# Kernel tuning notes

Hardware: AMD Instinct MI355X
Metric: run time of the kernel (lower is better)

Reference implementation:

```python
import jax, jax.numpy as jnp
import numpy as np

N, E = 20000, 320000
SQRT3 = float(np.sqrt(3.0))


def setup_inputs() -> dict:
    key = jax.random.key(0)
    ks = jax.random.split(key, 15)
    inp = {
        'node_features': jax.random.normal(ks[0], (N, 128), jnp.float32),
        'node_attrs': jax.random.uniform(ks[1], (N, 4), jnp.float32),
        'edge_attrs': jax.random.normal(ks[2], (E, 4), jnp.float32),
        'edge_embeddings': jax.random.uniform(ks[3], (E, 8), jnp.float32),
        'lin1_w0': jax.random.normal(ks[4], (32, 32), jnp.float32),
        'lin1_w1': jax.random.normal(ks[5], (32, 32), jnp.float32),
        'fc_w1': jax.random.normal(ks[6], (8, 64), jnp.float32),
        'fc_w2': jax.random.normal(ks[7], (64, 64), jnp.float32),
        'fc_w3': jax.random.normal(ks[8], (64, 128), jnp.float32),
        'lin2_w0': jax.random.normal(ks[9], (64, 64), jnp.float32),
        'lin2_w1': jax.random.normal(ks[10], (64, 32), jnp.float32),
        'sc_w0': jax.random.normal(ks[11], (32, 4, 64), jnp.float32),
        'sc_w1': jax.random.normal(ks[12], (32, 4, 32), jnp.float32),
        'edge_index': jax.random.randint(ks[13], (2, E), 0, N),
        'avg_num_neighbors': 16,
    }
    return inp


def reference(node_features, node_attrs, edge_attrs, edge_embeddings,
              lin1_w0, lin1_w1, fc_w1, fc_w2, fc_w3, lin2_w0, lin2_w1,
              sc_w0, sc_w1, edge_index, avg_num_neighbors):
    n = node_features.shape[0]
    src, dst = edge_index[0], edge_index[1]
    # split node features: 32x0e scalars + 32x1o vectors
    x0 = node_features[:, :32]                      # [N,32]
    x1 = node_features[:, 32:].reshape(n, 32, 3)    # [N,32,3]

    # self-connection: FullyConnectedTensorProduct with 4x0e node attrs ('uvw')
    sc_norm = 1.0 / np.sqrt(32 * 4)
    sc0 = jnp.einsum('nu,nv,uvw->nw', x0, node_attrs, sc_w0) * sc_norm   # [N,64]
    sc1 = jnp.einsum('nui,nv,uvw->nwi', x1, node_attrs, sc_w1) * sc_norm  # [N,32,3]

    # linear_1 (per-l equivariant linear, fan-in normalized)
    y0 = (x0 @ lin1_w0) / np.sqrt(32)
    y1 = jnp.einsum('nui,uw->nwi', x1, lin1_w1) / np.sqrt(32)

    # radial MLP -> per-edge TP weights (e3nn FullyConnectedNet: no bias, 1/sqrt(fan_in))
    h = jax.nn.silu((edge_embeddings @ fc_w1) / np.sqrt(8))
    h = jax.nn.silu((h @ fc_w2) / np.sqrt(64))
    w = (h @ fc_w3) / np.sqrt(64)                   # [E,128]
    # weights ordered by instruction: (0ex0e->0e),(0ex1o->1o),(1ox0e->1o),(1ox1o->0e)
    w00, w01, w10, w11 = w[:, :32], w[:, 32:64], w[:, 64:96], w[:, 96:128]

    # gather source node features per edge
    g0 = y0[src]                                    # [E,32]
    g1 = y1[src]                                    # [E,32,3]
    e0 = edge_attrs[:, :1]                          # [E,1]  (0e)
    e1 = edge_attrs[:, 1:4]                         # [E,3]  (1o)

    # sparse CG tensor product, 'uvu' with mul_v=1; output slots sorted as
    # [32x0e (0ex0e), 32x0e (1ox1o), 32x1o (0ex1o), 32x1o (1ox0e)]
    o_s0 = w00 * g0 * e0                                            # [E,32]
    o_s1 = w11 * jnp.einsum('eui,ei->eu', g1, e1) / SQRT3           # [E,32]
    o_v0 = (w01 * g0)[:, :, None] * e1[:, None, :]                  # [E,32,3]
    o_v1 = w10[:, :, None] * g1 * e0[:, :, None]                    # [E,32,3]
    edge_feat = jnp.concatenate(
        [o_s0, o_s1, o_v0.reshape(-1, 96), o_v1.reshape(-1, 96)], axis=1)  # [E,256]

    # scatter-sum into destination nodes
    m = jax.ops.segment_sum(edge_feat, dst, num_segments=n)
    m = m / np.sqrt(float(avg_num_neighbors))

    # linear_2: 64x0e+64x1o -> 64x0e+32x1o
    s0 = m[:, :64]
    s1 = m[:, 64:].reshape(n, 64, 3)
    out0 = (s0 @ lin2_w0) / np.sqrt(64) + sc0       # [N,64]
    out1 = jnp.einsum('nui,uw->nwi', s1, lin2_w1) / np.sqrt(64) + sc1  # [N,32,3]

    # Gate: 32x0e scalars (silu) + 32x0e gates (silu) acting on 32x1o
    scal = jax.nn.silu(out0[:, :32])
    gates = jax.nn.silu(out0[:, 32:])
    vec = gates[:, :, None] * out1                  # [N,32,3]
    new_x = jnp.concatenate([scal, vec.reshape(n, 96)], axis=1)  # [N,128]

    # resnet (irreps_layer_out == irreps_in)
    return node_features + new_x
```

## Files before the change

kernel.cpp:

```cpp
#include <hip/hip_runtime.h>
#include <math.h>

__device__ __forceinline__ float silu(float x) { return x / (1.0f + __expf(-x)); }

typedef __attribute__((ext_vector_type(8))) short short8v;
typedef __attribute__((ext_vector_type(4))) float f32x4;

__device__ __forceinline__ unsigned short f2bf(float x) {
  unsigned int u = __float_as_uint(x);
  return (unsigned short)((u + 0x8000u) >> 16);
}

__global__ __launch_bounds__(256) void node_pre_kernel(
    const float* __restrict__ nf, const float* __restrict__ na,
    const float* __restrict__ w0, const float* __restrict__ w1,
    const float* __restrict__ scw0, const float* __restrict__ scw1,
    float* __restrict__ y, float* __restrict__ sc, int N)
{
  __shared__ float nfL[32][132];
  __shared__ __align__(16) char aB[4096];
  __shared__ __align__(16) char wB[32768];
  const int t = threadIdx.x;
  const int n0 = blockIdx.x * 32;
  const int wv = t >> 6, l = t & 63;
  const int lrow = l & 15, lkg = l >> 4;
  const int ann = t >> 3, ac = t & 7;
  const float inv_sqrt32 = 0.17677669529663687f;
  const float sc_norm    = 0.08838834764831843f;

  for (int x4 = t; x4 < 1024; x4 += 256) {
    const int nn = x4 >> 5, c4 = x4 & 31;
    const int n = n0 + nn;
    float4 v = make_float4(0.f, 0.f, 0.f, 0.f);
    if (n < N) v = *(const float4*)(nf + (size_t)n * 128 + c4 * 4);
    *(float4*)&nfL[nn][c4 * 4] = v;
  }
  if (t < 128) {
    const int nn = t >> 2, c = t & 3;
    const int n = n0 + nn;
    nfL[nn][128 + c] = (n < N) ? na[(size_t)n * 4 + c] : 0.f;
  }
  for (int x = t; x < 1024; x += 256) {
    const int u = x >> 5, w = x & 31;
    *(unsigned short*)(wB + 0 + w * 128 + (((u >> 3) ^ (w & 7)) * 16) + (u & 7) * 2) = f2bf(w0[x]);
  }
  for (int x = t; x < 1024; x += 256) {
    const int u = x >> 5, w = x & 31;
    *(unsigned short*)(wB + 4096 + w * 128 + (((u >> 3) ^ (w & 7)) * 16) + (u & 7) * 2) = f2bf(w1[x]);
  }
  for (int x = t; x < 8192; x += 256) {
    const int k = x >> 6, c = x & 63;
    const int half = k >> 6, kk = k & 63;
    *(unsigned short*)(wB + 8192 + half * 8192 + c * 128 + (((kk >> 3) ^ (c & 7)) * 16) + (kk & 7) * 2) = f2bf(scw0[x]);
  }
  for (int x = t; x < 4096; x += 256) {
    const int k = x >> 5, c = x & 31;
    const int half = k >> 6, kk = k & 63;
    *(unsigned short*)(wB + 24576 + half * 4096 + c * 128 + (((kk >> 3) ^ (c & 7)) * 16) + (kk & 7) * 2) = f2bf(scw1[x]);
  }
  __syncthreads();

  if (ac < 4) {
    short8v hv;
#pragma unroll
    for (int j = 0; j < 8; ++j) hv[j] = (short)f2bf(nfL[ann][ac * 8 + j]);
    *(short8v*)(aB + ann * 128 + ((ac ^ (ann & 7)) * 16));
    *(short8v*)(aB + ann * 128 + ((ac ^ (ann & 7)) * 16)) = hv;
  }
  __syncthreads();
  {
    const int mt = wv >> 1, nt = wv & 1;
    const int ar = mt * 16 + lrow, br = nt * 16 + lrow;
    const short8v A = *(const short8v*)(aB + ar * 128 + ((lkg ^ (ar & 7)) * 16));
    const short8v B = *(const short8v*)(wB + 0 + br * 128 + ((lkg ^ (br & 7)) * 16));
    f32x4 acc = (f32x4){0.f, 0.f, 0.f, 0.f};
    acc = __builtin_amdgcn_mfma_f32_16x16x32_bf16(A, B, acc, 0, 0, 0);
#pragma unroll
    for (int r = 0; r < 4; ++r) {
      const int nn = mt * 16 + lkg * 4 + r;
      const int n = n0 + nn;
      if (n < N) y[(size_t)n * 128 + nt * 16 + lrow] = acc[r] * inv_sqrt32;
    }
  }
  __syncthreads();

  for (int i = 0; i < 3; ++i) {
    if (ac < 4) {
      short8v hv;
#pragma unroll
      for (int j = 0; j < 8; ++j)
        hv[j] = (short)f2bf(nfL[ann][32 + (ac * 8 + j) * 3 + i]);
      *(short8v*)(aB + ann * 128 + ((ac ^ (ann & 7)) * 16)) = hv;
    }
    __syncthreads();
    {
      const int mt = wv >> 1, nt = wv & 1;
      const int ar = mt * 16 + lrow, br = nt * 16 + lrow;
      const short8v A = *(const short8v*)(aB + ar * 128 + ((lkg ^ (ar & 7)) * 16));
      const short8v B = *(const short8v*)(wB + 4096 + br * 128 + ((lkg ^ (br & 7)) * 16));
      f32x4 acc = (f32x4){0.f, 0.f, 0.f, 0.f};
      acc = __builtin_amdgcn_mfma_f32_16x16x32_bf16(A, B, acc, 0, 0, 0);
#pragma unroll
      for (int r = 0; r < 4; ++r) {
        const int nn = mt * 16 + lkg * 4 + r;
        const int n = n0 + nn;
        if (n < N) y[(size_t)n * 128 + 32 + (nt * 16 + lrow) * 3 + i] = acc[r] * inv_sqrt32;
      }
    }
    __syncthreads();
  }

  {
    f32x4 accS[2] = {(f32x4){0.f,0.f,0.f,0.f}, (f32x4){0.f,0.f,0.f,0.f}};
    const int mt = wv & 1, ntb = (wv >> 1) * 2;
#pragma unroll
    for (int half = 0; half < 2; ++half) {
      {
        short8v hv;
#pragma unroll
        for (int j = 0; j < 8; ++j) {
          const int k = half * 64 + ac * 8 + j;
          hv[j] = (short)f2bf(nfL[ann][k >> 2] * nfL[ann][128 + (k & 3)]);
        }
        *(short8v*)(aB + ann * 128 + ((ac ^ (ann & 7)) * 16)) = hv;
      }
      __syncthreads();
#pragma unroll
      for (int step = 0; step < 2; ++step) {
        const int ar = mt * 16 + lrow;
        const short8v A = *(const short8v*)(aB + ar * 128 + (((step * 4 + lkg) ^ (ar & 7)) * 16));
#pragma unroll
        for (int q = 0; q < 2; ++q) {
          const int br = (ntb + q) * 16 + lrow;
          const short8v B = *(const short8v*)(wB + 8192 + half * 8192 + br * 128 + (((step * 4 + lkg) ^ (br & 7)) * 16));
          accS[q] = __builtin_amdgcn_mfma_f32_16x16x32_bf16(A, B, accS[q], 0, 0, 0);
        }
      }
      __syncthreads();
    }
#pragma unroll
    for (int q = 0; q < 2; ++q) {
#pragma unroll
      for (int r = 0; r < 4; ++r) {
        const int nn = mt * 16 + lkg * 4 + r;
        const int n = n0 + nn;
        if (n < N) sc[(size_t)n * 160 + (ntb + q) * 16 + lrow] = accS[q][r] * sc_norm;
      }
    }
  }

  for (int i = 0; i < 3; ++i) {
    f32x4 acc = (f32x4){0.f, 0.f, 0.f, 0.f};
    const int mt = wv >> 1, nt = wv & 1;
#pragma unroll
    for (int half = 0; half < 2; ++half) {
      {
        short8v hv;
#pragma unroll
        for (int j = 0; j < 8; ++j) {
          const int k = half * 64 + ac * 8 + j;
          hv[j] = (short)f2bf(nfL[ann][32 + (k >> 2) * 3 + i] * nfL[ann][128 + (k & 3)]);
        }
        *(short8v*)(aB + ann * 128 + ((ac ^ (ann & 7)) * 16)) = hv;
      }
      __syncthreads();
#pragma unroll
      for (int step = 0; step < 2; ++step) {
        const int ar = mt * 16 + lrow;
        const short8v A = *(const short8v*)(aB + ar * 128 + (((step * 4 + lkg) ^ (ar & 7)) * 16));
        const int br = nt * 16 + lrow;
        const short8v B = *(const short8v*)(wB + 24576 + half * 4096 + br * 128 + (((step * 4 + lkg) ^ (br & 7)) * 16));
        acc = __builtin_amdgcn_mfma_f32_16x16x32_bf16(A, B, acc, 0, 0, 0);
      }
      __syncthreads();
    }
#pragma unroll
    for (int r = 0; r < 4; ++r) {
      const int nn = mt * 16 + lkg * 4 + r;
      const int n = n0 + nn;
      if (n < N) sc[(size_t)n * 160 + 64 + (nt * 16 + lrow) * 3 + i] = acc[r] * sc_norm;
    }
  }
}

__global__ __launch_bounds__(256) void hist_kernel(const int* __restrict__ eidx,
                                                   int* __restrict__ counts, int E)
{
  const int e = blockIdx.x * 256 + threadIdx.x;
  if (e < E) atomicAdd(&counts[eidx[E + e]], 1);
}

__global__ __launch_bounds__(1024) void scan_kernel(const int* __restrict__ counts,
                                                    int* __restrict__ offsets,
                                                    int* __restrict__ cursor, int N)
{
  __shared__ int part[1024];
  const int t = threadIdx.x;
  const int per = (N + 1023) / 1024;
  const int base = t * per;
  int s = 0;
  for (int k = 0; k < per; ++k) { int idx = base + k; if (idx < N) s += counts[idx]; }
  part[t] = s;
  __syncthreads();
  for (int off = 1; off < 1024; off <<= 1) {
    int v = part[t];
    if (t >= off) v += part[t - off];
    __syncthreads();
    part[t] = v;
    __syncthreads();
  }
  int run = (t == 0) ? 0 : part[t - 1];
  for (int k = 0; k < per; ++k) {
    int idx = base + k;
    if (idx < N) { offsets[idx] = run; cursor[idx] = run; run += counts[idx]; }
  }
  if (t == 1023) offsets[N] = run;
}

__global__ __launch_bounds__(256) void scatter_kernel(const int* __restrict__ eidx,
                                                      int* __restrict__ cursor,
                                                      int* __restrict__ elist, int E)
{
  const int e = blockIdx.x * 256 + threadIdx.x;
  if (e >= E) return;
  const int dst = eidx[E + e];
  const int slot = atomicAdd(&cursor[dst], 1);
  elist[slot] = e;
}

__global__ __launch_bounds__(256) void edge_mlp_kernel(
    const float* __restrict__ eemb, const float* __restrict__ fw1,
    const float* __restrict__ fw2, const float* __restrict__ fw3,
    const int* __restrict__ elist, float* __restrict__ wbuf, int E)
{
  __shared__ __align__(16) float w1L[512];
  __shared__ __align__(16) char reg1[16384];
  __shared__ __align__(16) char reg2[32768];
  const int t = threadIdx.x;
  const int base = blockIdx.x * 128;

  for (int x = t; x < 512; x += 256)  w1L[x] = fw1[(x & 7) * 64 + (x >> 3)];
  for (int x = t; x < 4096; x += 256) {
    const int k = x >> 6, o = x & 63;
    *(unsigned short*)(reg2 + o * 128 + (((k >> 3) ^ (o & 7)) * 16) + (k & 7) * 2) = f2bf(fw2[x]);
  }

  const int e = t & 127, kg = t >> 7;
  {
    const int slot0 = base + e;
    const int eid = (slot0 < E) ? elist[slot0] : 0;
    const float4 em0 = *(const float4*)(eemb + (size_t)eid * 8);
    const float4 em1 = *(const float4*)(eemb + (size_t)eid * 8 + 4);
    __syncthreads();

    const float inv_sqrt8 = 0.35355339059327373f;
#pragma unroll
    for (int c = 0; c < 4; ++c) {
      short8v hv;
#pragma unroll
      for (int j = 0; j < 8; ++j) {
        const int k = kg * 32 + c * 8 + j;
        const float4 wa = *(const float4*)(w1L + k * 8);
        const float4 wb = *(const float4*)(w1L + k * 8 + 4);
        const float a = em0.x * wa.x + em0.y * wa.y + em0.z * wa.z + em0.w * wa.w
                      + em1.x * wb.x + em1.y * wb.y + em1.z * wb.z + em1.w * wb.w;
        hv[j] = (short)f2bf(silu(a * inv_sqrt8));
      }
      const int cc = kg * 4 + c;
      *(short8v*)(reg1 + e * 128 + ((cc ^ (e & 7)) * 16)) = hv;
    }
  }
  __syncthreads();

  const int wv = t >> 6, l = t & 63;
  const int lrow = l & 15, lkg = l >> 4;

  {
    f32x4 accB[2][4];
#pragma unroll
    for (int mt = 0; mt < 2; ++mt)
#pragma unroll
      for (int nt = 0; nt < 4; ++nt)
        accB[mt][nt] = (f32x4){0.f, 0.f, 0.f, 0.f};

#pragma unroll
    for (int step = 0; step < 2; ++step) {
#pragma unroll
      for (int mt = 0; mt < 2; ++mt) {
        const int ea = wv * 32 + mt * 16 + lrow;
        const short8v A = *(const short8v*)(reg1 + ea * 128 + (((step * 4 + lkg) ^ (ea & 7)) * 16));
#pragma unroll
        for (int nt = 0; nt < 4; ++nt) {
          const int o = nt * 16 + lrow;
          const short8v B = *(const short8v*)(reg2 + o * 128 + (((step * 4 + lkg) ^ (o & 7)) * 16));
          accB[mt][nt] = __builtin_amdgcn_mfma_f32_16x16x32_bf16(A, B, accB[mt][nt], 0, 0, 0);
        }
      }
    }
    __syncthreads();

#pragma unroll
    for (int mt = 0; mt < 2; ++mt) {
#pragma unroll
      for (int r = 0; r < 4; ++r) {
        const int eo = wv * 32 + mt * 16 + lkg * 4 + r;
#pragma unroll
        for (int nt = 0; nt < 4; ++nt) {
          const int o = nt * 16 + lrow;
          const float val = silu(accB[mt][nt][r] * 0.125f);
          *(unsigned short*)(reg1 + eo * 128 + (((o >> 3) ^ (eo & 7)) * 16) + (o & 7) * 2) = f2bf(val);
        }
      }
    }
  }
  for (int x = t; x < 8192; x += 256) {
    const int k = x >> 7, c = x & 127;
    *(unsigned short*)(reg2 + c * 128 + (((k >> 3) ^ (c & 7)) * 16) + (k & 7) * 2) = f2bf(fw3[x]);
  }
  __syncthreads();

  {
    f32x4 accd[2][8];
#pragma unroll
    for (int mt = 0; mt < 2; ++mt)
#pragma unroll
      for (int nt = 0; nt < 8; ++nt)
        accd[mt][nt] = (f32x4){0.f, 0.f, 0.f, 0.f};

#pragma unroll
    for (int step = 0; step < 2; ++step) {
      const int ea0 = wv * 32 + lrow;
      const int ea1 = wv * 32 + 16 + lrow;
      const short8v A0 = *(const short8v*)(reg1 + ea0 * 128 + (((step * 4 + lkg) ^ (ea0 & 7)) * 16));
      const short8v A1 = *(const short8v*)(reg1 + ea1 * 128 + (((step * 4 + lkg) ^ (ea1 & 7)) * 16));
#pragma unroll
      for (int nt = 0; nt < 8; ++nt) {
        const int n = nt * 16 + lrow;
        const short8v B = *(const short8v*)(reg2 + n * 128 + (((step * 4 + lkg) ^ (n & 7)) * 16));
        accd[0][nt] = __builtin_amdgcn_mfma_f32_16x16x32_bf16(A0, B, accd[0][nt], 0, 0, 0);
        accd[1][nt] = __builtin_amdgcn_mfma_f32_16x16x32_bf16(A1, B, accd[1][nt], 0, 0, 0);
      }
    }
#pragma unroll
    for (int mt = 0; mt < 2; ++mt) {
#pragma unroll
      for (int r = 0; r < 4; ++r) {
        const int eo = wv * 32 + mt * 16 + lkg * 4 + r;
        const int slot = base + eo;
        if (slot < E) {
          float* wrow = wbuf + (size_t)slot * 128 + lrow;
#pragma unroll
          for (int nt = 0; nt < 8; ++nt)
            wrow[nt * 16] = accd[mt][nt][r] * 0.125f;
        }
      }
    }
  }
}

__global__ __launch_bounds__(256) void gather_out_kernel(
    const float* __restrict__ nf, const float* __restrict__ wbuf,
    const float* __restrict__ y, const float* __restrict__ sc,
    const float* __restrict__ l2w0, const float* __restrict__ l2w1,
    const int* __restrict__ offsets, const int* __restrict__ elist,
    const int* __restrict__ eidx, const float* __restrict__ eattr,
    const int* __restrict__ avgp, float* __restrict__ out, int N, int E)
{
  __shared__ float mW[4][264];
  __shared__ float soW[4][160];
  const int t = threadIdx.x;
  const int wv = t >> 6, l = t & 63;
  const int n = blockIdx.x * 4 + wv;
  const bool valid = (n < N);
  const int u = l & 31, half = l >> 5;

  const int beg = valid ? offsets[n] : 0;
  const int end = valid ? offsets[n + 1] : 0;

  float s0 = 0.f, s1 = 0.f;
  float v0x = 0.f, v0y = 0.f, v0z = 0.f;
  float v1x = 0.f, v1y = 0.f, v1z = 0.f;

  for (int s = beg + half; s < end; s += 2) {
    const int eid = elist[s];
    const int src = eidx[eid];
    const float4 ea = *(const float4*)(eattr + (size_t)eid * 4);
    const float* wr = wbuf + (size_t)s * 128;
    const float* yr = y + (size_t)src * 128;
    const float w00 = wr[u], w01 = wr[32 + u], w10 = wr[64 + u], w11 = wr[96 + u];
    const float g0  = yr[u];
    const float g1x = yr[32 + 3 * u], g1y = yr[33 + 3 * u], g1z = yr[34 + 3 * u];
    s0 += w00 * g0 * ea.x;
    const float t01 = w01 * g0;
    v0x += t01 * ea.y; v0y += t01 * ea.z; v0z += t01 * ea.w;
    const float wg = w10 * ea.x;
    v1x += wg * g1x; v1y += wg * g1y; v1z += wg * g1z;
    s1 += w11 * (g1x * ea.y + g1y * ea.z + g1z * ea.w);
  }
  s0 += __shfl_xor(s0, 32);  s1 += __shfl_xor(s1, 32);
  v0x += __shfl_xor(v0x, 32); v0y += __shfl_xor(v0y, 32); v0z += __shfl_xor(v0z, 32);
  v1x += __shfl_xor(v1x, 32); v1y += __shfl_xor(v1y, 32); v1z += __shfl_xor(v1z, 32);
  if (half == 0) {
    mW[wv][u]          = s0;
    mW[wv][32 + u]     = s1 * 0.5773502691896258f;
    mW[wv][64 + 3 * u] = v0x; mW[wv][65 + 3 * u] = v0y; mW[wv][66 + 3 * u] = v0z;
    mW[wv][160 + 3 * u] = v1x; mW[wv][161 + 3 * u] = v1y; mW[wv][162 + 3 * u] = v1z;
  }
  __syncthreads();

  const float scl = 0.125f * rsqrtf((float)(*avgp));
  const float* m = mW[wv];
  if (valid) {
    {
      float acc = 0.f;
      for (int uu = 0; uu < 64; ++uu) acc += m[uu] * l2w0[uu * 64 + l];
      soW[wv][l] = acc * scl + sc[(size_t)n * 160 + l];
    }
    {
      const int w = l / 3, i = l - 3 * w;
      float acc = 0.f;
      for (int uu = 0; uu < 64; ++uu) acc += m[64 + uu * 3 + i] * l2w1[uu * 32 + w];
      soW[wv][64 + l] = acc * scl + sc[(size_t)n * 160 + 64 + l];
    }
    if (l < 32) {
      const int q = 64 + l, w = q / 3, i = q - 3 * w;
      float acc = 0.f;
      for (int uu = 0; uu < 64; ++uu) acc += m[64 + uu * 3 + i] * l2w1[uu * 32 + w];
      soW[wv][64 + q] = acc * scl + sc[(size_t)n * 160 + 64 + q];
    }
  }
  __syncthreads();

  if (valid) {
#pragma unroll
    for (int p = 0; p < 2; ++p) {
      const int c = p * 64 + l;
      float val;
      if (c < 32) {
        val = silu(soW[wv][c]);
      } else {
        const int q = c - 32, w = q / 3, i = q - 3 * w;
        val = silu(soW[wv][32 + w]) * soW[wv][64 + w * 3 + i];
      }
      out[(size_t)n * 128 + c] = nf[(size_t)n * 128 + c] + val;
    }
  }
}

extern "C" void kernel_launch(void* const* d_in, const int* in_sizes, int n_in,
                              void* d_out, int out_size, void* d_ws, size_t ws_size,
                              hipStream_t stream)
{
  const float* nf    = (const float*)d_in[0];
  const float* na    = (const float*)d_in[1];
  const float* eattr = (const float*)d_in[2];
  const float* eemb  = (const float*)d_in[3];
  const float* l1w0  = (const float*)d_in[4];
  const float* l1w1  = (const float*)d_in[5];
  const float* fw1   = (const float*)d_in[6];
  const float* fw2   = (const float*)d_in[7];
  const float* fw3   = (const float*)d_in[8];
  const float* l2w0  = (const float*)d_in[9];
  const float* l2w1  = (const float*)d_in[10];
  const float* scw0  = (const float*)d_in[11];
  const float* scw1  = (const float*)d_in[12];
  const int*   eidx  = (const int*)d_in[13];
  const int*   avgp  = (const int*)d_in[14];

  const int N = in_sizes[0] / 128;
  const int E = in_sizes[2] / 4;

  float* y       = (float*)d_ws;
  float* sc      = y + (size_t)N * 128;
  float* wbuf    = sc + (size_t)N * 160;
  int*   counts  = (int*)(wbuf + (size_t)E * 128);
  int*   offsets = counts + N;
  int*   cursor  = offsets + N + 1;
  int*   elist   = cursor + N;

  hipMemsetAsync(counts, 0, (size_t)N * sizeof(int), stream);
  node_pre_kernel<<<(N + 31) / 32, 256, 0, stream>>>(nf, na, l1w0, l1w1, scw0, scw1, y, sc, N);
  hist_kernel<<<(E + 255) / 256, 256, 0, stream>>>(eidx, counts, E);
  scan_kernel<<<1, 1024, 0, stream>>>(counts, offsets, cursor, N);
  scatter_kernel<<<(E + 255) / 256, 256, 0, stream>>>(eidx, cursor, elist, E);
  edge_mlp_kernel<<<(E + 127) / 128, 256, 0, stream>>>(eemb, fw1, fw2, fw3, elist, wbuf, E);
  gather_out_kernel<<<(N + 3) / 4, 256, 0, stream>>>(nf, wbuf, y, sc, l2w0, l2w1,
                                                     offsets, elist, eidx, eattr, avgp,
                                                     (float*)d_out, N, E);
}
```

Measured before the change: 223.3 us.

## Store per-edge TP weights as bf16 and prefetch next edge indices in gather

The per-edge weight buffer written by the edge MLP and read by the gather kernel is stored as bf16 instead of fp32, which halves the largest intermediate's write and read traffic (E×128 floats). The gather loop also software-pipelines the dependent elist→eidx→eattr loads for the next edge so they are in flight while the current edge is processed. A dead LDS read is removed. The bf16 rounding of the weights adds precision error to the result.

```diff
diff --git a/kernel.cpp b/kernel.cpp
--- a/kernel.cpp
+++ b/kernel.cpp
@@ -9,6 +9,9 @@
 __device__ __forceinline__ unsigned short f2bf(float x) {
   unsigned int u = __float_as_uint(x);
   return (unsigned short)((u + 0x8000u) >> 16);
+}
+__device__ __forceinline__ float bf2f(unsigned short v) {
+  return __uint_as_float(((unsigned int)v) << 16);
 }
 
 __global__ __launch_bounds__(256) void node_pre_kernel(
@@ -64,7 +67,6 @@
     short8v hv;
 #pragma unroll
     for (int j = 0; j < 8; ++j) hv[j] = (short)f2bf(nfL[ann][ac * 8 + j]);
-    *(short8v*)(aB + ann * 128 + ((ac ^ (ann & 7)) * 16));
     *(short8v*)(aB + ann * 128 + ((ac ^ (ann & 7)) * 16)) = hv;
   }
   __syncthreads();
@@ -231,7 +233,7 @@
 __global__ __launch_bounds__(256) void edge_mlp_kernel(
     const float* __restrict__ eemb, const float* __restrict__ fw1,
     const float* __restrict__ fw2, const float* __restrict__ fw3,
-    const int* __restrict__ elist, float* __restrict__ wbuf, int E)
+    const int* __restrict__ elist, unsigned short* __restrict__ wbuf, int E)
 {
   __shared__ __align__(16) float w1L[512];
   __shared__ __align__(16) char reg1[16384];
@@ -348,10 +350,10 @@
         const int eo = wv * 32 + mt * 16 + lkg * 4 + r;
         const int slot = base + eo;
         if (slot < E) {
-          float* wrow = wbuf + (size_t)slot * 128 + lrow;
+          unsigned short* wrow = wbuf + (size_t)slot * 128 + lrow;
 #pragma unroll
           for (int nt = 0; nt < 8; ++nt)
-            wrow[nt * 16] = accd[mt][nt][r] * 0.125f;
+            wrow[nt * 16] = f2bf(accd[mt][nt][r] * 0.125f);
         }
       }
     }
@@ -359,7 +361,7 @@
 }
 
 __global__ __launch_bounds__(256) void gather_out_kernel(
-    const float* __restrict__ nf, const float* __restrict__ wbuf,
+    const float* __restrict__ nf, const unsigned short* __restrict__ wbuf,
     const float* __restrict__ y, const float* __restrict__ sc,
     const float* __restrict__ l2w0, const float* __restrict__ l2w1,
     const int* __restrict__ offsets, const int* __restrict__ elist,
@@ -381,21 +383,34 @@
   float v0x = 0.f, v0y = 0.f, v0z = 0.f;
   float v1x = 0.f, v1y = 0.f, v1z = 0.f;
 
-  for (int s = beg + half; s < end; s += 2) {
+  int s = beg + half;
+  int srcC = 0; float4 eaC = make_float4(0.f, 0.f, 0.f, 0.f);
+  if (s < end) {
     const int eid = elist[s];
-    const int src = eidx[eid];
-    const float4 ea = *(const float4*)(eattr + (size_t)eid * 4);
-    const float* wr = wbuf + (size_t)s * 128;
-    const float* yr = y + (size_t)src * 128;
-    const float w00 = wr[u], w01 = wr[32 + u], w10 = wr[64 + u], w11 = wr[96 + u];
+    srcC = eidx[eid];
+    eaC = *(const float4*)(eattr + (size_t)eid * 4);
+  }
+  for (; s < end; ) {
+    const int s2 = s + 2;
+    int srcN = 0; float4 eaN = make_float4(0.f, 0.f, 0.f, 0.f);
+    if (s2 < end) {
+      const int eid2 = elist[s2];
+      srcN = eidx[eid2];
+      eaN = *(const float4*)(eattr + (size_t)eid2 * 4);
+    }
+    const unsigned short* wr = wbuf + (size_t)s * 128;
+    const float* yr = y + (size_t)srcC * 128;
+    const float w00 = bf2f(wr[u]),      w01 = bf2f(wr[32 + u]);
+    const float w10 = bf2f(wr[64 + u]), w11 = bf2f(wr[96 + u]);
     const float g0  = yr[u];
     const float g1x = yr[32 + 3 * u], g1y = yr[33 + 3 * u], g1z = yr[34 + 3 * u];
-    s0 += w00 * g0 * ea.x;
+    s0 += w00 * g0 * eaC.x;
     const float t01 = w01 * g0;
-    v0x += t01 * ea.y; v0y += t01 * ea.z; v0z += t01 * ea.w;
-    const float wg = w10 * ea.x;
+    v0x += t01 * eaC.y; v0y += t01 * eaC.z; v0z += t01 * eaC.w;
+    const float wg = w10 * eaC.x;
     v1x += wg * g1x; v1y += wg * g1y; v1z += wg * g1z;
-    s1 += w11 * (g1x * ea.y + g1y * ea.z + g1z * ea.w);
+    s1 += w11 * (g1x * eaC.y + g1y * eaC.z + g1z * eaC.w);
+    s = s2; srcC = srcN; eaC = eaN;
   }
   s0 += __shfl_xor(s0, 32);  s1 += __shfl_xor(s1, 32);
   v0x += __shfl_xor(v0x, 32); v0y += __shfl_xor(v0y, 32); v0z += __shfl_xor(v0z, 32);
@@ -472,8 +487,9 @@
 
   float* y       = (float*)d_ws;
   float* sc      = y + (size_t)N * 128;
-  float* wbuf    = sc + (size_t)N * 160;
-  int*   counts  = (int*)(wbuf + (size_t)E * 128);
+  float* wbuff   = sc + (size_t)N * 160;
+  unsigned short* wbuf = (unsigned short*)wbuff;
+  int*   counts  = (int*)(wbuff + (size_t)E * 128);
   int*   offsets = counts + N;
   int*   cursor  = offsets + N + 1;
   int*   elist   = cursor + N;
```

After: 215.9 us. -3.3%, faster.
